# Optimization experiments

Hardware: AMD Instinct MI355X
Metric: run time of the kernel (lower is better)

The kernel has to match this reference:

```python
import jax, jax.numpy as jnp
import numpy as np

BN_EPS = 1e-5

def setup_inputs() -> dict:
    key = jax.random.key(0)
    k1, k2, k3 = jax.random.split(key, 3)
    B, N, K, C, Cout = 8, 16384, 16, 128, 256
    x = jax.random.normal(k1, (B, N, C), dtype=jnp.float32)
    edge_index = jax.random.randint(k2, (B, N, K), 0, N, dtype=jnp.int64)
    W = jax.random.normal(k3, (Cout, 2 * C), dtype=jnp.float32) * (1.0 / np.sqrt(2 * C))
    b = jnp.zeros((Cout,), dtype=jnp.float32)
    gamma = jnp.ones((Cout,), dtype=jnp.float32)
    beta = jnp.zeros((Cout,), dtype=jnp.float32)
    return {"x": x, "edge_index": edge_index, "W": W, "b": b, "gamma": gamma, "beta": beta}

def reference(x, edge_index, W, b, gamma, beta):
    B, N, C = x.shape
    # gather neighbors: [B, N, K, C]
    neighbors = x[jnp.arange(B)[:, None, None], edge_index]
    # max-relative aggregation: max_j x_j - x_i
    agg = neighbors.max(axis=2) - x                      # [B, N, C]
    h = jnp.concatenate([x, agg], axis=-1).reshape(B * N, 2 * C)
    y = h @ W.T + b                                      # Linear -> [B*N, Cout]
    # BatchNorm1d (training mode: batch statistics, biased variance)
    mean = y.mean(axis=0)
    var = y.var(axis=0)
    y = (y - mean) * jax.lax.rsqrt(var + BN_EPS) * gamma + beta
    out = jax.nn.gelu(y, approximate=False)
    return out.reshape(B, N, -1)
```

## Files before the change

### kernel.cpp

```cpp
#include <hip/hip_runtime.h>
#include <math.h>

constexpr int B_ = 8;
constexpr int N_ = 16384;
constexpr int C_ = 128;
constexpr int K_ = 16;
constexpr int CO = 256;
constexpr int TC = 256;
constexpr int M_ = B_ * N_;
constexpr int TM = 64;
constexpr int NB = M_ / TM;
constexpr int NCHUNK = 8;

typedef _Float16 h8 __attribute__((ext_vector_type(8)));
typedef float f4 __attribute__((ext_vector_type(4)));

__device__ __forceinline__ float4 f4max(float4 a, float4 b) {
  return make_float4(fmaxf(a.x, b.x), fmaxf(a.y, b.y),
                     fmaxf(a.z, b.z), fmaxf(a.w, b.w));
}

__device__ __forceinline__ ushort4 pack_h4(float4 v) {
  union { _Float16 h[4]; ushort4 u; } cv;
  cv.h[0] = (_Float16)v.x; cv.h[1] = (_Float16)v.y;
  cv.h[2] = (_Float16)v.z; cv.h[3] = (_Float16)v.w;
  return cv.u;
}

__device__ __forceinline__ uint4 hmax4(uint4 a, uint4 b) {
  union U { uint4 u; _Float16 h[8]; } ua, ub, r;
  ua.u = a; ub.u = b;
  #pragma unroll
  for (int i = 0; i < 8; ++i) r.h[i] = ua.h[i] > ub.h[i] ? ua.h[i] : ub.h[i];
  return r.u;
}

__device__ __forceinline__ uint4 hsub4(uint4 a, uint4 b) {
  union U { uint4 u; _Float16 h[8]; } ua, ub, r;
  ua.u = a; ub.u = b;
  #pragma unroll
  for (int i = 0; i < 8; ++i) r.h[i] = ua.h[i] - ub.h[i];
  return r.u;
}

__device__ __forceinline__ float gelu_f(float u) {
  float z = fabsf(u) * 0.70710678118654752f;
  float t = 1.0f / (1.0f + 0.3275911f * z);
  float p = t * (0.254829592f + t * (-0.284496736f + t * (1.421413741f +
            t * (-1.453152027f + t * 1.061405429f))));
  float erfz = 1.0f - p * __expf(-z * z);
  erfz = copysignf(erfz, u);
  return 0.5f * u * (1.0f + erfz);
}

__global__ void k0_prep(const float* __restrict__ W, _Float16* __restrict__ Wf) {
  int g = blockIdx.x * 256 + threadIdx.x;
  int cout = g >> 5;
  int G = g & 31;
  int kk = G >> 2, go = G & 3;
  int nt = cout >> 4, c15 = cout & 15;
  const float* src = W + (size_t)cout * TC + G * 8;
  _Float16* dst = Wf + kk * 8192 + nt * 512 + (c15 + 16 * go) * 8;
  #pragma unroll
  for (int j = 0; j < 8; ++j) dst[j] = (_Float16)src[j];
}

__global__ __launch_bounds__(256)
void k0b_cvt(const float* __restrict__ x, _Float16* __restrict__ xh) {
  const size_t total = (size_t)M_ * C_ / 4;
  const size_t stride = (size_t)gridDim.x * 256;
  for (size_t i = (size_t)blockIdx.x * 256 + threadIdx.x; i < total; i += stride) {
    float4 a = ((const float4*)x)[i];
    ((ushort4*)xh)[i] = pack_h4(a);
  }
}

template <int FP16>
__global__ __launch_bounds__(256, 4)
void k1_fused(const float* __restrict__ x, const int* __restrict__ eidx,
              const _Float16* __restrict__ Wf, const float* __restrict__ bias,
              float* __restrict__ y, double* __restrict__ stats,
              const _Float16* __restrict__ xh)
{
  __shared__ __align__(16) _Float16 hsf[TM * TC];
  __shared__ __align__(16) int ids[TM * K_];

  const int tid = threadIdx.x;
  const int wave = tid >> 6;
  const int lane = tid & 63;
  const int batch = blockIdx.x & 7;
  const int tile = blockIdx.x >> 3;
  const long long row0 = (long long)batch * N_ + (long long)tile * TM;

  ((int4*)ids)[tid] = ((const int4*)(eidx + row0 * K_))[tid];
  __syncthreads();

  if constexpr (FP16) {
    const _Float16* __restrict__ xbh = xh + (size_t)batch * N_ * C_;
    #pragma unroll
    for (int it = 0; it < 4; ++it) {
      int w = it * 256 + tid;
      int m = w >> 4;
      int ch8 = (w & 15) << 3;
      uint4 xv = *(const uint4*)(xh + (row0 + m) * (size_t)C_ + ch8);
      uint4 mx = *(const uint4*)(xbh + (size_t)ids[m * K_] * C_ + ch8);
      #pragma unroll
      for (int j = 1; j < K_; ++j) {
        int nb = ids[m * K_ + j];
        mx = hmax4(mx, *(const uint4*)(xbh + (size_t)nb * C_ + ch8));
      }
      uint4 dv = hsub4(mx, xv);
      int a0 = ((m >> 4) << 13) | ((ch8 >> 3) << 8) | ((m & 15) << 4);
      a0 ^= ((a0 >> 8) & 7) << 4;
      *(uint4*)((char*)hsf + a0) = xv;
      int c2 = 128 + ch8;
      int a1 = ((m >> 4) << 13) | ((c2 >> 3) << 8) | ((m & 15) << 4);
      a1 ^= ((a1 >> 8) & 7) << 4;
      *(uint4*)((char*)hsf + a1) = dv;
    }
  } else {
    const float* __restrict__ xb = x + (size_t)batch * N_ * C_;
    #pragma unroll
    for (int it = 0; it < 8; ++it) {
      int w = it * 256 + tid;
      int m = w >> 5;
      int cq = (w & 31) << 2;
      float4 xv = *(const float4*)(x + (row0 + m) * (size_t)C_ + cq);
      float4 mx = make_float4(-INFINITY, -INFINITY, -INFINITY, -INFINITY);
      #pragma unroll
      for (int j = 0; j < K_; ++j) {
        int nb = ids[m * K_ + j];
        mx = f4max(mx, *(const float4*)(xb + (size_t)nb * C_ + cq));
      }
      int a0 = ((m >> 4) << 13) | ((cq >> 3) << 8) | ((m & 15) << 4) | ((cq & 4) << 1);
      a0 ^= ((a0 >> 8) & 7) << 4;
      *(ushort4*)((char*)hsf + a0) = pack_h4(xv);
      float4 dv = make_float4(mx.x - xv.x, mx.y - xv.y, mx.z - xv.z, mx.w - xv.w);
      int c2 = 128 + cq;
      int a1 = ((m >> 4) << 13) | ((c2 >> 3) << 8) | ((m & 15) << 4) | ((cq & 4) << 1);
      a1 ^= ((a1 >> 8) & 7) << 4;
      *(ushort4*)((char*)hsf + a1) = pack_h4(dv);
    }
  }
  __syncthreads();

  f4 acc[4][4] = {};
  #pragma unroll
  for (int kk = 0; kk < NCHUNK; ++kk) {
    h8 af[4], bf[4];
    #pragma unroll
    for (int nt = 0; nt < 4; ++nt)
      bf[nt] = *(const h8*)((const char*)Wf + (kk << 14) + (wave << 12) + (nt << 10) + (lane << 4));
    #pragma unroll
    for (int mt = 0; mt < 4; ++mt) {
      int off = (mt << 13) + (kk << 10) + lane * 16;
      off ^= ((off >> 8) & 7) << 4;
      af[mt] = *(const h8*)((const char*)hsf + off);
    }
    #pragma unroll
    for (int mt = 0; mt < 4; ++mt)
      #pragma unroll
      for (int nt = 0; nt < 4; ++nt)
        acc[mt][nt] = __builtin_amdgcn_mfma_f32_16x16x32_f16(af[mt], bf[nt], acc[mt][nt], 0, 0, 0);
  }

  const int c15 = lane & 15;
  const int rg = lane >> 4;
  float s4[4] = {0.f, 0.f, 0.f, 0.f};
  float q4[4] = {0.f, 0.f, 0.f, 0.f};
  #pragma unroll
  for (int nt = 0; nt < 4; ++nt) {
    int col = (wave << 6) + (nt << 4) + c15;
    float bb = bias[col];
    #pragma unroll
    for (int mt = 0; mt < 4; ++mt) {
      #pragma unroll
      for (int r = 0; r < 4; ++r) {
        float v = acc[mt][nt][r] + bb;
        long long row = row0 + (mt << 4) + (rg << 2) + r;
        y[row * CO + col] = v;
        s4[nt] += v;
        q4[nt] += v * v;
      }
    }
  }
  #pragma unroll
  for (int nt = 0; nt < 4; ++nt) {
    s4[nt] += __shfl_xor(s4[nt], 16, 64);
    s4[nt] += __shfl_xor(s4[nt], 32, 64);
    q4[nt] += __shfl_xor(q4[nt], 16, 64);
    q4[nt] += __shfl_xor(q4[nt], 32, 64);
  }
  if (lane < 16) {
    #pragma unroll
    for (int nt = 0; nt < 4; ++nt) {
      int col = (wave << 6) + (nt << 4) + c15;
      atomicAdd(&stats[col], (double)s4[nt]);
      atomicAdd(&stats[col + 256], (double)q4[nt]);
    }
  }
}

__global__ void k2_stats(const double* __restrict__ stats,
                         const float* __restrict__ gamma,
                         const float* __restrict__ beta,
                         float* __restrict__ ss) {
  int c = threadIdx.x;
  double mean = stats[c] * (1.0 / M_);
  double var  = stats[256 + c] * (1.0 / M_) - mean * mean;
  double scale = (double)gamma[c] / sqrt(var + 1e-5);
  ss[c]       = (float)scale;
  ss[256 + c] = (float)((double)beta[c] - mean * scale);
}

__global__ __launch_bounds__(256)
void k3_bn_gelu(float* __restrict__ y, const float* __restrict__ ss) {
  size_t i = (size_t)blockIdx.x * blockDim.x + threadIdx.x;
  const size_t stride = (size_t)gridDim.x * blockDim.x;
  const size_t total = (size_t)M_ * CO / 4;
  int c4 = (int)(i & (CO / 4 - 1)) * 4;
  float4 sc = *(const float4*)(ss + c4);
  float4 sh = *(const float4*)(ss + 256 + c4);
  float4* y4 = (float4*)y;
  for (; i < total; i += stride) {
    float4 v = y4[i];
    float4 r;
    r.x = gelu_f(v.x * sc.x + sh.x);
    r.y = gelu_f(v.y * sc.y + sh.y);
    r.z = gelu_f(v.z * sc.z + sh.z);
    r.w = gelu_f(v.w * sc.w + sh.w);
    y4[i] = r;
  }
}

extern "C" void kernel_launch(void* const* d_in, const int* in_sizes, int n_in,
                              void* d_out, int out_size, void* d_ws, size_t ws_size,
                              hipStream_t stream)
{
  const float* x     = (const float*)d_in[0];
  const int*   eidx  = (const int*)d_in[1];
  const float* W     = (const float*)d_in[2];
  const float* bias  = (const float*)d_in[3];
  const float* gamma = (const float*)d_in[4];
  const float* beta  = (const float*)d_in[5];
  float* y = (float*)d_out;
  char* ws = (char*)d_ws;

  _Float16* Wf    = (_Float16*)ws;
  double*   stats = (double*)(ws + 131072);
  float*    ss    = (float*)(ws + 131072 + 4096);
  _Float16* xh    = (_Float16*)(ws + (1 << 20));
  const size_t ws_needed = (1 << 20) + (size_t)M_ * C_ * 2;
  const bool fp16path = ws_size >= ws_needed;

  (void)hipMemsetAsync(stats, 0, 512 * sizeof(double), stream);
  k0_prep<<<32, 256, 0, stream>>>(W, Wf);
  if (fp16path) {
    k0b_cvt<<<2048, 256, 0, stream>>>(x, xh);
    k1_fused<1><<<NB, 256, 0, stream>>>(x, eidx, Wf, bias, y, stats, xh);
  } else {
    k1_fused<0><<<NB, 256, 0, stream>>>(x, eidx, Wf, bias, y, stats, nullptr);
  }
  k2_stats<<<1, 256, 0, stream>>>(stats, gamma, beta, ss);
  k3_bn_gelu<<<2048, 256, 0, stream>>>(y, ss);
}
```

Baseline: 296.6 us.

## Merge prep kernels and fold BN stats finalize into GELU kernel

Combines the weight conversion, stats zeroing and x-to-fp16 conversion into one launch, replacing a memset and two kernels. It folds the stats-to-scale/shift computation into the BN+GELU kernel, with each thread recomputing its four channels in double, and doubles that kernel's grid. The neighbor gather in the fused kernel now uses 32-bit byte offsets instead of 64-bit index arithmetic. The aim is lower launch overhead and less address math, at the cost of redundant per-thread double-precision stats work.

```diff
diff --git a/kernel.cpp b/kernel.cpp
--- a/kernel.cpp
+++ b/kernel.cpp
@@ -53,25 +53,31 @@
   return 0.5f * u * (1.0f + erfz);
 }
 
-__global__ void k0_prep(const float* __restrict__ W, _Float16* __restrict__ Wf) {
-  int g = blockIdx.x * 256 + threadIdx.x;
-  int cout = g >> 5;
-  int G = g & 31;
-  int kk = G >> 2, go = G & 3;
-  int nt = cout >> 4, c15 = cout & 15;
-  const float* src = W + (size_t)cout * TC + G * 8;
-  _Float16* dst = Wf + kk * 8192 + nt * 512 + (c15 + 16 * go) * 8;
-  #pragma unroll
-  for (int j = 0; j < 8; ++j) dst[j] = (_Float16)src[j];
-}
-
 __global__ __launch_bounds__(256)
-void k0b_cvt(const float* __restrict__ x, _Float16* __restrict__ xh) {
-  const size_t total = (size_t)M_ * C_ / 4;
-  const size_t stride = (size_t)gridDim.x * 256;
-  for (size_t i = (size_t)blockIdx.x * 256 + threadIdx.x; i < total; i += stride) {
-    float4 a = ((const float4*)x)[i];
-    ((ushort4*)xh)[i] = pack_h4(a);
+void kA_prep(const float* __restrict__ W, _Float16* __restrict__ Wf,
+             const float* __restrict__ x, _Float16* __restrict__ xh,
+             double* __restrict__ stats)
+{
+  const int bid = blockIdx.x;
+  const int tid = threadIdx.x;
+  if (bid < 32) {
+    int g = bid * 256 + tid;
+    int cout = g >> 5;
+    int G = g & 31;
+    int kk = G >> 2, go = G & 3;
+    int nt = cout >> 4, c15 = cout & 15;
+    const float* src = W + (size_t)cout * TC + G * 8;
+    _Float16* dst = Wf + kk * 8192 + nt * 512 + (c15 + 16 * go) * 8;
+    #pragma unroll
+    for (int j = 0; j < 8; ++j) dst[j] = (_Float16)src[j];
+  } else if (bid == 32) {
+    stats[tid] = 0.0;
+    stats[256 + tid] = 0.0;
+  } else if (xh != nullptr) {
+    const size_t total = (size_t)M_ * C_ / 4;
+    const size_t stride = (size_t)2048 * 256;
+    for (size_t i = (size_t)(bid - 33) * 256 + tid; i < total; i += stride)
+      ((ushort4*)xh)[i] = pack_h4(((const float4*)x)[i]);
   }
 }
 
@@ -96,18 +102,20 @@
   __syncthreads();
 
   if constexpr (FP16) {
-    const _Float16* __restrict__ xbh = xh + (size_t)batch * N_ * C_;
+    const char* __restrict__ xb8 = (const char*)(xh + (size_t)batch * N_ * C_);
     #pragma unroll
     for (int it = 0; it < 4; ++it) {
       int w = it * 256 + tid;
       int m = w >> 4;
       int ch8 = (w & 15) << 3;
-      uint4 xv = *(const uint4*)(xh + (row0 + m) * (size_t)C_ + ch8);
-      uint4 mx = *(const uint4*)(xbh + (size_t)ids[m * K_] * C_ + ch8);
+      unsigned co = (unsigned)(ch8 << 1);
+      unsigned self = ((unsigned)(unsigned long long)(row0 + m) << 8) + co;
+      uint4 xv = *(const uint4*)((const char*)xh + self);
+      uint4 mx = *(const uint4*)(xb8 + (((unsigned)ids[m * K_] << 8) + co));
       #pragma unroll
       for (int j = 1; j < K_; ++j) {
-        int nb = ids[m * K_ + j];
-        mx = hmax4(mx, *(const uint4*)(xbh + (size_t)nb * C_ + ch8));
+        unsigned off = ((unsigned)ids[m * K_ + j] << 8) + co;
+        mx = hmax4(mx, *(const uint4*)(xb8 + off));
       }
       uint4 dv = hsub4(mx, xv);
       int a0 = ((m >> 4) << 13) | ((ch8 >> 3) << 8) | ((m & 15) << 4);
@@ -201,34 +209,32 @@
   }
 }
 
-__global__ void k2_stats(const double* __restrict__ stats,
-                         const float* __restrict__ gamma,
-                         const float* __restrict__ beta,
-                         float* __restrict__ ss) {
-  int c = threadIdx.x;
-  double mean = stats[c] * (1.0 / M_);
-  double var  = stats[256 + c] * (1.0 / M_) - mean * mean;
-  double scale = (double)gamma[c] / sqrt(var + 1e-5);
-  ss[c]       = (float)scale;
-  ss[256 + c] = (float)((double)beta[c] - mean * scale);
-}
-
 __global__ __launch_bounds__(256)
-void k3_bn_gelu(float* __restrict__ y, const float* __restrict__ ss) {
+void kB_bn_gelu(float* __restrict__ y, const double* __restrict__ stats,
+                const float* __restrict__ gamma, const float* __restrict__ beta)
+{
+  const int c4 = (threadIdx.x & 63) * 4;
+  float sc[4], sh[4];
+  #pragma unroll
+  for (int j = 0; j < 4; ++j) {
+    int c = c4 + j;
+    double mean = stats[c] * (1.0 / M_);
+    double var  = stats[256 + c] * (1.0 / M_) - mean * mean;
+    double scale = (double)gamma[c] / sqrt(var + 1e-5);
+    sc[j] = (float)scale;
+    sh[j] = (float)((double)beta[c] - mean * scale);
+  }
   size_t i = (size_t)blockIdx.x * blockDim.x + threadIdx.x;
   const size_t stride = (size_t)gridDim.x * blockDim.x;
   const size_t total = (size_t)M_ * CO / 4;
-  int c4 = (int)(i & (CO / 4 - 1)) * 4;
-  float4 sc = *(const float4*)(ss + c4);
-  float4 sh = *(const float4*)(ss + 256 + c4);
   float4* y4 = (float4*)y;
   for (; i < total; i += stride) {
     float4 v = y4[i];
     float4 r;
-    r.x = gelu_f(v.x * sc.x + sh.x);
-    r.y = gelu_f(v.y * sc.y + sh.y);
-    r.z = gelu_f(v.z * sc.z + sh.z);
-    r.w = gelu_f(v.w * sc.w + sh.w);
+    r.x = gelu_f(v.x * sc[0] + sh[0]);
+    r.y = gelu_f(v.y * sc[1] + sh[1]);
+    r.z = gelu_f(v.z * sc[2] + sh[2]);
+    r.w = gelu_f(v.w * sc[3] + sh[3]);
     y4[i] = r;
   }
 }
@@ -248,19 +254,15 @@
 
   _Float16* Wf    = (_Float16*)ws;
   double*   stats = (double*)(ws + 131072);
-  float*    ss    = (float*)(ws + 131072 + 4096);
   _Float16* xh    = (_Float16*)(ws + (1 << 20));
   const size_t ws_needed = (1 << 20) + (size_t)M_ * C_ * 2;
   const bool fp16path = ws_size >= ws_needed;
 
-  (void)hipMemsetAsync(stats, 0, 512 * sizeof(double), stream);
-  k0_prep<<<32, 256, 0, stream>>>(W, Wf);
+  kA_prep<<<2081, 256, 0, stream>>>(W, Wf, x, fp16path ? xh : nullptr, stats);
   if (fp16path) {
-    k0b_cvt<<<2048, 256, 0, stream>>>(x, xh);
     k1_fused<1><<<NB, 256, 0, stream>>>(x, eidx, Wf, bias, y, stats, xh);
   } else {
     k1_fused<0><<<NB, 256, 0, stream>>>(x, eidx, Wf, bias, y, stats, nullptr);
   }
-  k2_stats<<<1, 256, 0, stream>>>(stats, gamma, beta, ss);
-  k3_bn_gelu<<<2048, 256, 0, stream>>>(y, ss);
-}
+  kB_bn_gelu<<<4096, 256, 0, stream>>>(y, stats, gamma, beta);
+}
```

Result: faster. 289.5 us (-2.4%).
